# Performance work log

Measured on AMD Instinct MI355X. Metric: run time of the kernel, lower is better.

The kernel has to match this reference:

```python
import jax, jax.numpy as jnp
import numpy as np

D_ORIG, D_HEAD, N_HEAD = 64, 32, 8
D_EMB = D_HEAD * N_HEAD


def setup_inputs() -> dict:
    key = jax.random.key(0)
    ks = jax.random.split(key, 9)
    b, l = 1, 512
    x = jax.random.normal(ks[0], (b, l, D_ORIG), dtype=jnp.float32)
    e = jax.random.normal(ks[1], (b, l, l, D_ORIG), dtype=jnp.float32)
    s = 1.0 / np.sqrt(D_ORIG)
    Wq = jax.random.uniform(ks[2], (D_ORIG, D_EMB), jnp.float32, -s, s)
    Wk = jax.random.uniform(ks[3], (D_ORIG, D_EMB), jnp.float32, -s, s)
    Wv = jax.random.uniform(ks[4], (D_ORIG, D_EMB), jnp.float32, -s, s)
    We = jax.random.uniform(ks[5], (D_ORIG, D_EMB), jnp.float32, -s, s)
    so = 1.0 / np.sqrt(D_EMB)
    Wo = jax.random.uniform(ks[6], (D_EMB, D_ORIG), jnp.float32, -so, so)
    bo = jax.random.uniform(ks[7], (D_ORIG,), jnp.float32, -so, so)
    return {"x": x, "e": e, "Wq": Wq, "Wk": Wk, "Wv": Wv, "We": We, "Wo": Wo, "bo": bo}


def reference(x, e, Wq, Wk, Wv, We, Wo, bo):
    b, l, _ = x.shape
    # projections
    q = (x @ Wq).reshape(b, l, N_HEAD, D_HEAD).transpose(0, 2, 1, 3)  # b n l d
    k = (x @ Wk).reshape(b, l, N_HEAD, D_HEAD).transpose(0, 2, 1, 3)
    v = (x @ Wv).reshape(b, l, N_HEAD, D_HEAD).transpose(0, 2, 1, 3)
    ee = (e @ We).reshape(b, l, l, N_HEAD, D_HEAD).transpose(0, 3, 1, 2, 4)  # b n i j d
    # edge-biased keys/values: broadcast add over query index i
    kb = k[:, :, None, :, :] + ee  # b n i j d
    logit = jnp.einsum('bnid,bnijd->bnij', q, kb) * (D_HEAD ** -0.5)
    attn = jax.nn.softmax(logit, axis=-1)
    vb = v[:, :, None, :, :] + ee  # b n i j d
    out = jnp.einsum('bnij,bnijd->bnid', attn, vb)  # b n i d
    out = out.transpose(0, 2, 1, 3).reshape(b, l, D_EMB)
    return out @ Wo + bo
```

## Files before the change

### kernel.cpp

```cpp
#include <hip/hip_runtime.h>

#define SCALE 0.17677669529663687f

__global__ __launch_bounds__(256) void coef_kernel(
    const float* __restrict__ x, const float* __restrict__ Wq,
    const float* __restrict__ Wk, const float* __restrict__ We,
    float* __restrict__ qc_ws) {
  const int t = threadIdx.x, i = blockIdx.x;
  __shared__ float s_x[64], s_q[256];
  if (t < 64) s_x[t] = x[i * 64 + t];
  __syncthreads();
  float a = 0;
#pragma unroll 8
  for (int c = 0; c < 64; ++c) a += s_x[c] * Wq[c * 256 + t];
  s_q[t] = a * SCALE;
  __syncthreads();
  const int c = t >> 2, hb = (t & 3) * 4;
  const float* W = (hb < 8) ? We : Wk;
  float o4[4];
#pragma unroll
  for (int u = 0; u < 4; ++u) {
    int n = (hb + u) & 7;
    const float* wrow = W + c * 256 + n * 32;
    const float* qrow = s_q + n * 32;
    float s = 0;
#pragma unroll
    for (int d = 0; d < 32; ++d) s += qrow[d] * wrow[d];
    o4[u] = s;
  }
#pragma unroll
  for (int u = 0; u < 4; ++u) qc_ws[i * 1024 + t * 4 + u] = o4[u];
}

__global__ __launch_bounds__(512, 4) void attn_kernel(
    const float* __restrict__ e, const float* __restrict__ x,
    const float* __restrict__ qc_ws,
    const float* __restrict__ We, const float* __restrict__ Wv,
    const float* __restrict__ Wo, const float* __restrict__ bo,
    float* __restrict__ out) {
  const int t = threadIdx.x, i = blockIdx.x;
  __shared__ __align__(16) float s_qc[1024];
  __shared__ __align__(16) float s_p[8 * 512];
  __shared__ __align__(16) float s_part[8 * 1024];
  __shared__ float s_ae[512], s_px[512];
  __shared__ float s_emb[256];
  __shared__ float s_op[8 * 64];

  s_qc[t] = qc_ws[i * 1024 + t];
  s_qc[t + 512] = qc_ws[i * 1024 + 512 + t];
  __syncthreads();

  const int c4 = t & 15;
  const int strip = t >> 4;
  const float4* e4 = (const float4*)(e + (size_t)i * 512 * 64);
  const float4* x4 = (const float4*)x;

  float ce[4][8], cx[4][8];
#pragma unroll
  for (int cc = 0; cc < 4; ++cc) {
    const int cb = (c4 * 4 + cc) * 16;
#pragma unroll
    for (int h = 0; h < 8; ++h) { ce[cc][h] = s_qc[cb + h]; cx[cc][h] = s_qc[cb + 8 + h]; }
  }

  {
    const int j0 = strip * 16;
    float4 E = e4[j0 * 16 + c4];
    float4 X = x4[j0 * 16 + c4];
    for (int jj = 0; jj < 16; ++jj) {
      const int j = j0 + jj;
      float4 En, Xn;
      if (jj < 15) { En = e4[(j + 1) * 16 + c4]; Xn = x4[(j + 1) * 16 + c4]; }
      float acc[8];
#pragma unroll
      for (int h = 0; h < 8; ++h)
        acc[h] = E.x * ce[0][h] + E.y * ce[1][h] + E.z * ce[2][h] + E.w * ce[3][h]
               + X.x * cx[0][h] + X.y * cx[1][h] + X.z * cx[2][h] + X.w * cx[3][h];
#pragma unroll
      for (int m = 1; m <= 8; m <<= 1) {
#pragma unroll
        for (int h = 0; h < 8; ++h) acc[h] += __shfl_xor(acc[h], m, 64);
      }
      if (c4 == 0) {
#pragma unroll
        for (int h = 0; h < 8; ++h) s_p[h * 512 + j] = acc[h];
      }
      E = En; X = Xn;
    }
  }
  __syncthreads();

  {
    const int n = t >> 6, l64 = t & 63;
    float m = -1e30f;
#pragma unroll
    for (int u = 0; u < 8; ++u) m = fmaxf(m, s_p[n * 512 + l64 + u * 64]);
#pragma unroll
    for (int off = 32; off; off >>= 1) m = fmaxf(m, __shfl_xor(m, off, 64));
    float sum = 0;
#pragma unroll
    for (int u = 0; u < 8; ++u) {
      float p = __expf(s_p[n * 512 + l64 + u * 64] - m);
      s_p[n * 512 + l64 + u * 64] = p;
      sum += p;
    }
#pragma unroll
    for (int off = 32; off; off >>= 1) sum += __shfl_xor(sum, off, 64);
    const float inv = 1.0f / sum;
#pragma unroll
    for (int u = 0; u < 8; ++u) s_p[n * 512 + l64 + u * 64] *= inv;
  }
  __syncthreads();

  {
    float ae[4][8], px[4][8];
#pragma unroll
    for (int cc = 0; cc < 4; ++cc)
#pragma unroll
      for (int h = 0; h < 8; ++h) { ae[cc][h] = 0.f; px[cc][h] = 0.f; }
    const int j0 = strip * 16;
    float4 E = e4[j0 * 16 + c4];
    float4 X = x4[j0 * 16 + c4];
    for (int jj = 0; jj < 16; ++jj) {
      const int j = j0 + jj;
      float4 En, Xn;
      if (jj < 15) { En = e4[(j + 1) * 16 + c4]; Xn = x4[(j + 1) * 16 + c4]; }
      float pr[8];
#pragma unroll
      for (int h = 0; h < 8; ++h) pr[h] = s_p[h * 512 + j];
#pragma unroll
      for (int h = 0; h < 8; ++h) {
        ae[0][h] += pr[h] * E.x; ae[1][h] += pr[h] * E.y;
        ae[2][h] += pr[h] * E.z; ae[3][h] += pr[h] * E.w;
        px[0][h] += pr[h] * X.x; px[1][h] += pr[h] * X.y;
        px[2][h] += pr[h] * X.z; px[3][h] += pr[h] * X.w;
      }
      E = En; X = Xn;
    }
#pragma unroll
    for (int m = 16; m <= 32; m <<= 1) {
#pragma unroll
      for (int cc = 0; cc < 4; ++cc)
#pragma unroll
        for (int h = 0; h < 8; ++h) {
          ae[cc][h] += __shfl_xor(ae[cc][h], m, 64);
          px[cc][h] += __shfl_xor(px[cc][h], m, 64);
        }
    }
    const int wv = t >> 6;
    if ((t & 48) == 0) {
#pragma unroll
      for (int h = 0; h < 8; ++h) {
        *(float4*)&s_part[wv * 1024 + h * 64 + c4 * 4] =
            make_float4(ae[0][h], ae[1][h], ae[2][h], ae[3][h]);
        *(float4*)&s_part[wv * 1024 + 512 + h * 64 + c4 * 4] =
            make_float4(px[0][h], px[1][h], px[2][h], px[3][h]);
      }
    }
  }
  __syncthreads();

  {
    float va = 0, vp = 0;
#pragma unroll
    for (int w = 0; w < 8; ++w) {
      va += s_part[w * 1024 + t];
      vp += s_part[w * 1024 + 512 + t];
    }
    s_ae[t] = va; s_px[t] = vp;
  }
  __syncthreads();

  {
    const int nd = t & 255, ch = t >> 8, hn = nd >> 5;
    float emb = 0;
    const int cb = ch * 32;
#pragma unroll 8
    for (int c = cb; c < cb + 32; ++c)
      emb += s_ae[hn * 64 + c] * We[c * 256 + nd] + s_px[hn * 64 + c] * Wv[c * 256 + nd];
    s_part[ch * 256 + nd] = emb;
  }
  __syncthreads();
  if (t < 256) s_emb[t] = s_part[t] + s_part[256 + t];
  __syncthreads();
  {
    const int o = t & 63, mc = t >> 6;
    float oo = 0;
#pragma unroll 8
    for (int m2 = mc * 32; m2 < mc * 32 + 32; ++m2) oo += s_emb[m2] * Wo[m2 * 64 + o];
    s_op[mc * 64 + o] = oo;
  }
  __syncthreads();
  if (t < 64) {
    float r = bo[t];
#pragma unroll
    for (int w = 0; w < 8; ++w) r += s_op[w * 64 + t];
    out[i * 64 + t] = r;
  }
}

extern "C" void kernel_launch(void* const* d_in, const int* in_sizes, int n_in,
                              void* d_out, int out_size, void* d_ws, size_t ws_size,
                              hipStream_t stream) {
  const float* x  = (const float*)d_in[0];
  const float* e  = (const float*)d_in[1];
  const float* Wq = (const float*)d_in[2];
  const float* Wk = (const float*)d_in[3];
  const float* Wv = (const float*)d_in[4];
  const float* We = (const float*)d_in[5];
  const float* Wo = (const float*)d_in[6];
  const float* bo = (const float*)d_in[7];
  float* out = (float*)d_out;

  float* qc_ws = (float*)d_ws;

  hipLaunchKernelGGL(coef_kernel, dim3(512), dim3(256), 0, stream,
                     x, Wq, Wk, We, qc_ws);
  hipLaunchKernelGGL(attn_kernel, dim3(512), dim3(512), 0, stream,
                     e, x, qc_ws, We, Wv, Wo, bo, out);
}
```

Measured before the change: 162.6 us.

## Fuse coefficient kernel into attention kernel and use transpose-reduce for logits

Folds the query-coefficient projection into the attention kernel so it is computed per block, which removes one launch and the workspace round-trip. The per-row logit reduction swaps the full 8-head butterfly (32 shuffles) for a recursive-halving exchange that needs fewer shuffles. The probability buffer is padded to a stride of 513 to reduce LDS bank conflicts. The manual software prefetch of e and x is replaced by full unrolling, and the coefficient dot products are vectorised with float4. Risks include higher register pressure from unrolling and redundant We/Wk reads per block.

```diff
diff --git a/kernel.cpp b/kernel.cpp
--- a/kernel.cpp
+++ b/kernel.cpp
@@ -1,53 +1,48 @@
 #include <hip/hip_runtime.h>
 
 #define SCALE 0.17677669529663687f
-
-__global__ __launch_bounds__(256) void coef_kernel(
-    const float* __restrict__ x, const float* __restrict__ Wq,
-    const float* __restrict__ Wk, const float* __restrict__ We,
-    float* __restrict__ qc_ws) {
-  const int t = threadIdx.x, i = blockIdx.x;
-  __shared__ float s_x[64], s_q[256];
-  if (t < 64) s_x[t] = x[i * 64 + t];
-  __syncthreads();
-  float a = 0;
-#pragma unroll 8
-  for (int c = 0; c < 64; ++c) a += s_x[c] * Wq[c * 256 + t];
-  s_q[t] = a * SCALE;
-  __syncthreads();
-  const int c = t >> 2, hb = (t & 3) * 4;
-  const float* W = (hb < 8) ? We : Wk;
-  float o4[4];
-#pragma unroll
-  for (int u = 0; u < 4; ++u) {
-    int n = (hb + u) & 7;
-    const float* wrow = W + c * 256 + n * 32;
-    const float* qrow = s_q + n * 32;
-    float s = 0;
-#pragma unroll
-    for (int d = 0; d < 32; ++d) s += qrow[d] * wrow[d];
-    o4[u] = s;
-  }
-#pragma unroll
-  for (int u = 0; u < 4; ++u) qc_ws[i * 1024 + t * 4 + u] = o4[u];
-}
-
-__global__ __launch_bounds__(512, 4) void attn_kernel(
+#define PSTR 513
+
+__global__ __launch_bounds__(512, 4) void fused_kernel(
     const float* __restrict__ e, const float* __restrict__ x,
-    const float* __restrict__ qc_ws,
+    const float* __restrict__ Wq, const float* __restrict__ Wk,
     const float* __restrict__ We, const float* __restrict__ Wv,
     const float* __restrict__ Wo, const float* __restrict__ bo,
     float* __restrict__ out) {
   const int t = threadIdx.x, i = blockIdx.x;
+  __shared__ float s_x[64];
+  __shared__ __align__(16) float s_q[256];
   __shared__ __align__(16) float s_qc[1024];
-  __shared__ __align__(16) float s_p[8 * 512];
+  __shared__ __align__(16) float s_p[8 * PSTR];
   __shared__ __align__(16) float s_part[8 * 1024];
   __shared__ float s_ae[512], s_px[512];
   __shared__ float s_emb[256];
   __shared__ float s_op[8 * 64];
 
-  s_qc[t] = qc_ws[i * 1024 + t];
-  s_qc[t + 512] = qc_ws[i * 1024 + 512 + t];
+  if (t < 64) s_x[t] = x[i * 64 + t];
+  __syncthreads();
+  if (t < 256) {
+    float a = 0;
+#pragma unroll 8
+    for (int c = 0; c < 64; ++c) a += s_x[c] * Wq[c * 256 + t];
+    s_q[t] = a * SCALE;
+  }
+  __syncthreads();
+  {
+    const int c = t >> 3, h = t & 7;
+    const float4* wer = (const float4*)(We + c * 256 + h * 32);
+    const float4* wkr = (const float4*)(Wk + c * 256 + h * 32);
+    const float4* qr = (const float4*)(s_q + h * 32);
+    float se = 0, sk = 0;
+#pragma unroll
+    for (int u = 0; u < 8; ++u) {
+      float4 w1 = wer[u], w2 = wkr[u], qv = qr[u];
+      se += qv.x * w1.x + qv.y * w1.y + qv.z * w1.z + qv.w * w1.w;
+      sk += qv.x * w2.x + qv.y * w2.y + qv.z * w2.z + qv.w * w2.w;
+    }
+    s_qc[c * 16 + h] = se;
+    s_qc[c * 16 + 8 + h] = sk;
+  }
   __syncthreads();
 
   const int c4 = t & 15;
@@ -65,27 +60,36 @@
 
   {
     const int j0 = strip * 16;
-    float4 E = e4[j0 * 16 + c4];
-    float4 X = x4[j0 * 16 + c4];
+#pragma unroll
     for (int jj = 0; jj < 16; ++jj) {
       const int j = j0 + jj;
-      float4 En, Xn;
-      if (jj < 15) { En = e4[(j + 1) * 16 + c4]; Xn = x4[(j + 1) * 16 + c4]; }
+      float4 E = e4[j * 16 + c4];
+      float4 X = x4[j * 16 + c4];
       float acc[8];
 #pragma unroll
       for (int h = 0; h < 8; ++h)
         acc[h] = E.x * ce[0][h] + E.y * ce[1][h] + E.z * ce[2][h] + E.w * ce[3][h]
                + X.x * cx[0][h] + X.y * cx[1][h] + X.z * cx[2][h] + X.w * cx[3][h];
-#pragma unroll
-      for (int m = 1; m <= 8; m <<= 1) {
-#pragma unroll
-        for (int h = 0; h < 8; ++h) acc[h] += __shfl_xor(acc[h], m, 64);
-      }
-      if (c4 == 0) {
-#pragma unroll
-        for (int h = 0; h < 8; ++h) s_p[h * 512 + j] = acc[h];
-      }
-      E = En; X = Xn;
+      float a4[4];
+#pragma unroll
+      for (int u = 0; u < 4; ++u) {
+        float sent = (c4 & 8) ? acc[u] : acc[4 + u];
+        float kept = (c4 & 8) ? acc[4 + u] : acc[u];
+        a4[u] = kept + __shfl_xor(sent, 8, 64);
+      }
+      float a2[2];
+#pragma unroll
+      for (int u = 0; u < 2; ++u) {
+        float sent = (c4 & 4) ? a4[u] : a4[2 + u];
+        float kept = (c4 & 4) ? a4[2 + u] : a4[u];
+        a2[u] = kept + __shfl_xor(sent, 4, 64);
+      }
+      float sent = (c4 & 2) ? a2[0] : a2[1];
+      float kept = (c4 & 2) ? a2[1] : a2[0];
+      float a1 = kept + __shfl_xor(sent, 2, 64);
+      a1 += __shfl_xor(a1, 1, 64);
+      const int h = c4 >> 1;
+      if (!(c4 & 1)) s_p[h * PSTR + j] = a1;
     }
   }
   __syncthreads();
@@ -94,21 +98,21 @@
     const int n = t >> 6, l64 = t & 63;
     float m = -1e30f;
 #pragma unroll
-    for (int u = 0; u < 8; ++u) m = fmaxf(m, s_p[n * 512 + l64 + u * 64]);
+    for (int u = 0; u < 8; ++u) m = fmaxf(m, s_p[n * PSTR + l64 + u * 64]);
 #pragma unroll
     for (int off = 32; off; off >>= 1) m = fmaxf(m, __shfl_xor(m, off, 64));
     float sum = 0;
 #pragma unroll
     for (int u = 0; u < 8; ++u) {
-      float p = __expf(s_p[n * 512 + l64 + u * 64] - m);
-      s_p[n * 512 + l64 + u * 64] = p;
+      float p = __expf(s_p[n * PSTR + l64 + u * 64] - m);
+      s_p[n * PSTR + l64 + u * 64] = p;
       sum += p;
     }
 #pragma unroll
     for (int off = 32; off; off >>= 1) sum += __shfl_xor(sum, off, 64);
     const float inv = 1.0f / sum;
 #pragma unroll
-    for (int u = 0; u < 8; ++u) s_p[n * 512 + l64 + u * 64] *= inv;
+    for (int u = 0; u < 8; ++u) s_p[n * PSTR + l64 + u * 64] *= inv;
   }
   __syncthreads();
 
@@ -119,15 +123,14 @@
 #pragma unroll
       for (int h = 0; h < 8; ++h) { ae[cc][h] = 0.f; px[cc][h] = 0.f; }
     const int j0 = strip * 16;
-    float4 E = e4[j0 * 16 + c4];
-    float4 X = x4[j0 * 16 + c4];
+#pragma unroll
     for (int jj = 0; jj < 16; ++jj) {
       const int j = j0 + jj;
-      float4 En, Xn;
-      if (jj < 15) { En = e4[(j + 1) * 16 + c4]; Xn = x4[(j + 1) * 16 + c4]; }
+      float4 E = e4[j * 16 + c4];
+      float4 X = x4[j * 16 + c4];
       float pr[8];
 #pragma unroll
-      for (int h = 0; h < 8; ++h) pr[h] = s_p[h * 512 + j];
+      for (int h = 0; h < 8; ++h) pr[h] = s_p[h * PSTR + j];
 #pragma unroll
       for (int h = 0; h < 8; ++h) {
         ae[0][h] += pr[h] * E.x; ae[1][h] += pr[h] * E.y;
@@ -135,7 +138,6 @@
         px[0][h] += pr[h] * X.x; px[1][h] += pr[h] * X.y;
         px[2][h] += pr[h] * X.z; px[3][h] += pr[h] * X.w;
       }
-      E = En; X = Xn;
     }
 #pragma unroll
     for (int m = 16; m <= 32; m <<= 1) {
@@ -212,10 +214,6 @@
   const float* bo = (const float*)d_in[7];
   float* out = (float*)d_out;
 
-  float* qc_ws = (float*)d_ws;
-
-  hipLaunchKernelGGL(coef_kernel, dim3(512), dim3(256), 0, stream,
-                     x, Wq, Wk, We, qc_ws);
-  hipLaunchKernelGGL(attn_kernel, dim3(512), dim3(512), 0, stream,
-                     e, x, qc_ws, We, Wv, Wo, bo, out);
+  hipLaunchKernelGGL(fused_kernel, dim3(512), dim3(512), 0, stream,
+                     e, x, Wq, Wk, We, Wv, Wo, bo, out);
 }
```

Result: slower. 182.4 us (+12.2%).
